# Kernel optimization log

Measured on AMD Instinct MI355X. Metric: run time of the kernel, lower is better.

The kernel has to match this reference:

```python
import jax, jax.numpy as jnp
import numpy as np

LSTM_SIZE = 64
NUM_OPS = 5
NUM_LAYERS = 7  # 2 warmup anchors + 5 sampled layers (layer_id 2..6)


def _lstm_cell(x, h, c, w_ih, w_hh, b_ih, b_hh):
    # torch LSTMCell gate order: i, f, g, o
    g = x @ w_ih.T + b_ih + h @ w_hh.T + b_hh  # [1, 4*64]
    i, f, gg, o = jnp.split(g, 4, axis=1)
    c2 = jax.nn.sigmoid(f) * c + jax.nn.sigmoid(i) * jnp.tanh(gg)
    h2 = jax.nn.sigmoid(o) * jnp.tanh(c2)
    return h2, c2


def _sampler(embed, w_ih, w_hh, b_ih, b_hh, w_soft, b_soft, b_soft_no_learn,
             w_attn1, w_attn2, v_attn, prev_c, prev_h, use_bias, key):
    keys = jax.random.split(key, 20)  # 5 layers * (2 index + 2 op) samples
    k = 0
    anchors, anchors_w1, arc_seq = [], [], []
    log_prob = jnp.float32(0.0)
    entropy = jnp.float32(0.0)
    inputs = embed[0][None, :]
    # warmup: two anchor slots (anchors are zeros, per original code)
    for _ in range(2):
        prev_h, prev_c = _lstm_cell(inputs, prev_h, prev_c, w_ih, w_hh, b_ih, b_hh)
        anchors.append(jnp.zeros((1, LSTM_SIZE), jnp.float32))
        anchors_w1.append(prev_h @ w_attn1.T)
    for layer_id in range(2, NUM_LAYERS):
        idxs, ops = [], []
        # sample 2 previous-layer indices via tiny attention
        for _ in range(2):
            prev_h, prev_c = _lstm_cell(inputs, prev_h, prev_c, w_ih, w_hh, b_ih, b_hh)
            query = jnp.concatenate(anchors_w1, axis=0)            # [layer_id, 64]
            q = jnp.tanh(query + prev_h @ w_attn2.T)               # broadcast [layer_id, 64]
            logits = (q @ v_attn.T).reshape(layer_id)              # [layer_id]
            logits = logits / 5.0 + 1.1 * jnp.tanh(logits)
            index = jax.random.categorical(keys[k], logits); k += 1
            logp = jax.nn.log_softmax(logits)
            log_prob = log_prob + (-logp[index])
            entropy = entropy + jax.lax.stop_gradient(-jnp.sum(logp * jnp.exp(logp)))
            idxs.append(index)
            A = jnp.concatenate(anchors, axis=0)                   # [layer_id, 64]
            inputs = A[index][None, :]
        # sample 2 ops
        for _ in range(2):
            prev_h, prev_c = _lstm_cell(inputs, prev_h, prev_c, w_ih, w_hh, b_ih, b_hh)
            logits = (prev_h @ w_soft.T + b_soft)                  # [1, 5]
            logits = 1.1 / 2.5 * jnp.tanh(logits / 5.0)
            if use_bias:
                logits = logits + b_soft_no_learn
            logits = logits[0]
            op_id = jax.random.categorical(keys[k], logits); k += 1
            logp = jax.nn.log_softmax(logits)
            log_prob = log_prob + (-logp[op_id])
            entropy = entropy + jax.lax.stop_gradient(-jnp.sum(logp * jnp.exp(logp)))
            ops.append(op_id)
            inputs = embed[op_id + 1][None, :]
        # extra step producing this layer's anchor
        prev_h, prev_c = _lstm_cell(inputs, prev_h, prev_c, w_ih, w_hh, b_ih, b_hh)
        anchors.append(prev_h)
        anchors_w1.append(prev_h @ w_attn1.T)
        inputs = embed[0][None, :]
        # arc layout per layer after in-place fixups: [idx1, op1, idx2, op2]
        arc_seq += [idxs[0], ops[0], idxs[1], ops[1]]
    arc = jnp.stack(arc_seq)
    return arc, entropy, log_prob, prev_c, prev_h


def setup_inputs() -> dict:
    key = jax.random.key(0)
    ks = jax.random.split(key, 9)
    u = lambda k, shape: jax.random.uniform(k, shape, jnp.float32, -0.1, 0.1)
    return {
        "embed": u(ks[0], (6, LSTM_SIZE)),
        "w_ih": u(ks[1], (4 * LSTM_SIZE, LSTM_SIZE)),
        "w_hh": u(ks[2], (4 * LSTM_SIZE, LSTM_SIZE)),
        "b_ih": u(ks[3], (4 * LSTM_SIZE,)),
        "b_hh": u(ks[4], (4 * LSTM_SIZE,)),
        "w_soft": u(ks[5], (NUM_OPS, LSTM_SIZE)),
        "b_soft": jnp.array([[10.0, 10.0, 0.0, 0.0, 0.0]], jnp.float32),
        "b_soft_no_learn": jnp.array([[0.25, 0.25, -0.25, -0.25, -0.25]], jnp.float32),
        "w_attn1": u(ks[6], (LSTM_SIZE, LSTM_SIZE)),
        "w_attn2": u(ks[7], (LSTM_SIZE, LSTM_SIZE)),
        "v_attn": u(ks[8], (1, LSTM_SIZE)),
        "seed": 0,
    }


def reference(embed, w_ih, w_hh, b_ih, b_hh, w_soft, b_soft, b_soft_no_learn,
              w_attn1, w_attn2, v_attn, seed):
    key = jax.random.key(seed)
    k1, k2 = jax.random.split(key)
    zc = jnp.zeros((1, LSTM_SIZE), jnp.float32)
    zh = jnp.zeros((1, LSTM_SIZE), jnp.float32)
    arc1, ent1, lp1, c, h = _sampler(embed, w_ih, w_hh, b_ih, b_hh, w_soft, b_soft,
                                     b_soft_no_learn, w_attn1, w_attn2, v_attn,
                                     zc, zh, True, k1)
    arc2, ent2, lp2, _, _ = _sampler(embed, w_ih, w_hh, b_ih, b_hh, w_soft, b_soft,
                                     b_soft_no_learn, w_attn1, w_attn2, v_attn,
                                     c, h, False, k2)
    return (arc1, arc2, lp1 + lp2, ent1 + ent2)
```

## Files before the change

### kernel.cpp

```cpp
#include <hip/hip_runtime.h>
#include <cstdint>

#ifndef FASTMATH
#define FASTMATH 1
#endif

#define NT 512

__device__ __forceinline__ uint32_t rotl32_(uint32_t v, int d) {
  return (v << d) | (v >> (32 - d));
}

__device__ __forceinline__ void tf2x32(uint32_t k0, uint32_t k1,
                                       uint32_t x0, uint32_t x1,
                                       uint32_t& o0, uint32_t& o1) {
  const uint32_t k2 = k0 ^ k1 ^ 0x1BD11BDAu;
  x0 += k0; x1 += k1;
#define TF4(a,b,c,d) \
  x0 += x1; x1 = rotl32_(x1,a); x1 ^= x0; \
  x0 += x1; x1 = rotl32_(x1,b); x1 ^= x0; \
  x0 += x1; x1 = rotl32_(x1,c); x1 ^= x0; \
  x0 += x1; x1 = rotl32_(x1,d); x1 ^= x0;
  TF4(13,15,26,6)
  x0 += k1; x1 += k2 + 1u;
  TF4(17,29,16,24)
  x0 += k2; x1 += k0 + 2u;
  TF4(13,15,26,6)
  x0 += k0; x1 += k1 + 3u;
  TF4(17,29,16,24)
  x0 += k1; x1 += k2 + 4u;
  TF4(13,15,26,6)
  x0 += k2; x1 += k0 + 5u;
#undef TF4
  o0 = x0; o1 = x1;
}

#if FASTMATH
__device__ __forceinline__ float tanh_(float x) {
  float e = __expf(2.0f * x);
  return 1.0f - __fdividef(2.0f, e + 1.0f);
}
__device__ __forceinline__ float sig_(float x) {
  return __fdividef(1.0f, 1.0f + __expf(-x));
}
#define log_ __logf
#define exp_ __expf
#else
__device__ __forceinline__ float tanh_(float x) { return tanhf(x); }
__device__ __forceinline__ float sig_(float x) { return 0.5f * tanhf(0.5f * x) + 0.5f; }
#define log_ logf
#define exp_ expf
#endif

template <int CTRL>
__device__ __forceinline__ float dppf(float x) {
  return __int_as_float(__builtin_amdgcn_update_dpp(
      0, __float_as_int(x), CTRL, 0xF, 0xF, true));
}
template <int CTRL>
__device__ __forceinline__ int dppi(int x) {
  return __builtin_amdgcn_update_dpp(0, x, CTRL, 0xF, 0xF, true);
}
constexpr int QP1 = 0xB1;
constexpr int QP2 = 0x4E;
constexpr int HM  = 0x141;

__global__ __launch_bounds__(NT, 2)
void nas_controller(const float* __restrict__ embed,
                    const float* __restrict__ w_ih,
                    const float* __restrict__ w_hh,
                    const float* __restrict__ b_ih,
                    const float* __restrict__ b_hh,
                    const float* __restrict__ w_soft,
                    const float* __restrict__ b_soft,
                    const float* __restrict__ b_soft_nl,
                    const float* __restrict__ w_attn1,
                    const float* __restrict__ w_attn2,
                    const float* __restrict__ v_attn,
                    const int* __restrict__ seedp,
                    float* __restrict__ out) {
  const int tid  = threadIdx.x;
  const int lane = tid & 63;
  const int wid  = tid >> 6;

  const int hh   = lane & 1;
  const int role = (lane >> 1) & 3;
  const int ul   = lane >> 3;
  const int u    = (wid << 3) | ul;
  const int rblk = (0x3120 >> (4 * role)) & 0xF;
  const int refrow = rblk * 64 + u;

  __shared__ __align__(16) float attn1L[64 * 68];
  __shared__ __align__(16) float attn2L[64 * 68];
  __shared__ __align__(16) float wsoftL[5 * 68];
  __shared__ __align__(16) float aw1sF[7 * 68];
  __shared__ __align__(16) float hw2[64];
  __shared__ __align__(16) float hL[2][64];
  __shared__ __align__(16) float preL[13 * 256];
  __shared__ float gL[320];
  __shared__ float vaL[64];
  __shared__ float bsoftL[8], bnlL[8];
  __shared__ int   seliL;

  for (int i4 = tid; i4 < 1024; i4 += NT) {
    int r = i4 >> 4, c4 = i4 & 15;
    reinterpret_cast<float4*>(attn1L)[r * 17 + c4] =
        reinterpret_cast<const float4*>(w_attn1)[i4];
    reinterpret_cast<float4*>(attn2L)[r * 17 + c4] =
        reinterpret_cast<const float4*>(w_attn2)[i4];
  }
  if (tid < 320) { int r = tid >> 6, c = tid & 63; wsoftL[r * 68 + c] = w_soft[tid]; }
  if (tid < 64) { vaL[tid] = v_attn[tid]; hL[0][tid] = 0.f; hL[1][tid] = 0.f; }
  if (tid < 8) {
    bsoftL[tid] = (tid < 5) ? b_soft[tid] : 0.f;
    bnlL[tid]   = (tid < 5) ? b_soft_nl[tid] : 0.f;
  }
  for (int i = tid; i < 512; i += NT) preL[6 * 256 + i] = 0.f;

  if (tid < 320) {
    int s = tid >= 160 ? 1 : 0;
    int rem = tid - s * 160;
    int k = rem >> 3, i = rem & 7;
    uint32_t a, b, ka, kb, o0, o1;
    tf2x32(0u, (uint32_t)seedp[0], 0u, (uint32_t)s, a, b);
    tf2x32(a, b, 0u, (uint32_t)k, ka, kb);
    tf2x32(ka, kb, 0u, (uint32_t)i, o0, o1);
    uint32_t bits = o0 ^ o1;
    const float TINY = 1.1754943508222875e-38f;
    float uu = __uint_as_float((bits >> 9) | 0x3f800000u) - 1.0f;
    uu = uu * (1.0f - TINY) + TINY;
    uu = fmaxf(TINY, uu);
    gL[tid] = -log_(-log_(uu));
  }

  float4 wi[8], wh[8];
  {
    const float4* a = reinterpret_cast<const float4*>(w_ih) + refrow * 16 + hh * 8;
#pragma unroll
    for (int j = 0; j < 8; ++j) wi[j] = a[j];
    const float4* b = reinterpret_cast<const float4*>(w_hh) + refrow * 16 + hh * 8;
#pragma unroll
    for (int j = 0; j < 8; ++j) wh[j] = b[j];
  }
  const float bsum = b_ih[refrow] + b_hh[refrow];

#pragma unroll
  for (int e = 0; e < 6; ++e) {
    const float4* x4 = reinterpret_cast<const float4*>(embed) + e * 16 + hh * 8;
    float ax = 0, ay = 0, az = 0, aw = 0;
#pragma unroll
    for (int j = 0; j < 8; ++j) {
      float4 x = x4[j], w = wi[j];
      ax = fmaf(w.x, x.x, ax); ay = fmaf(w.y, x.y, ay);
      az = fmaf(w.z, x.z, az); aw = fmaf(w.w, x.w, aw);
    }
    float acc = (ax + ay) + (az + aw);
    float tot = acc + dppf<QP1>(acc);
    if (hh == 0) preL[e * 256 + u * 4 + role] = tot;
  }

  int curH = 0, srcSlot = 0;
  float creg = 0.f;
  float lp = 0.f, ent = 0.f;

  auto lstm = [&]() {
    __syncthreads();
    const float4* h4 = reinterpret_cast<const float4*>(hL[curH]) + hh * 8;
    float ax = 0, ay = 0, az = 0, aw = 0;
#pragma unroll
    for (int j = 0; j < 8; ++j) {
      float4 x = h4[j], w = wh[j];
      ax = fmaf(w.x, x.x, ax); ay = fmaf(w.y, x.y, ay);
      az = fmaf(w.z, x.z, az); aw = fmaf(w.w, x.w, aw);
    }
    float acc = (ax + ay) + (az + aw);
    if (hh == 0) acc += preL[srcSlot * 256 + u * 4 + role] + bsum;
    float gs = acc + dppf<QP1>(acc);
    float nl = (role == 1) ? tanh_(gs) : sig_(gs);
    float other = dppf<QP2>(nl);
    float P = (lane & 4) ? (((role == 2) ? nl : other) * creg)
                         : (nl * other);
    float c2 = P + dppf<HM>(P);
    creg = c2;
    if (role == 3 && hh == 0) hL[curH ^ 1][u] = nl * tanh_(c2);
    curH ^= 1;
  };

  auto matvec = [&](const float* Wl, float* dst) {
    const int r = tid >> 3, q = tid & 7;
    const float4* w4 = reinterpret_cast<const float4*>(Wl + r * 68) + q * 2;
    float4 wa = w4[0], wb = w4[1];
    const float4* h4 = reinterpret_cast<const float4*>(hL[curH]) + q * 2;
    float4 ha = h4[0], hb = h4[1];
    float acc = fmaf(wa.x, ha.x, fmaf(wa.y, ha.y, fmaf(wa.z, ha.z, wa.w * ha.w)));
    acc += fmaf(wb.x, hb.x, fmaf(wb.y, hb.y, fmaf(wb.z, hb.z, wb.w * hb.w)));
    acc += dppf<QP1>(acc); acc += dppf<QP2>(acc); acc += dppf<HM>(acc);
    if (q == 0) dst[r] = acc;
  };

  auto anchorPre = [&](int slot) {
    const float4* h4 = reinterpret_cast<const float4*>(hL[curH]) + hh * 8;
    float ax = 0, ay = 0, az = 0, aw = 0;
#pragma unroll
    for (int j = 0; j < 8; ++j) {
      float4 x = h4[j], w = wi[j];
      ax = fmaf(w.x, x.x, ax); ay = fmaf(w.y, x.y, ay);
      az = fmaf(w.z, x.z, az); aw = fmaf(w.w, x.w, aw);
    }
    float acc = (ax + ay) + (az + aw);
    float tot = acc + dppf<QP1>(acc);
    if (hh == 0) preL[slot * 256 + u * 4 + role] = tot;
  };

  int sIdx = 0;
  auto doSample = [&](int n, int k, int mode, float raw, float* op) {
    float l;
    if (lane < n) {
      if (mode == 0) l = raw / 5.0f + 1.1f * tanh_(raw);
      else {
        l = (float)(1.1 / 2.5) * tanh_(raw / 5.0f);
        if (mode == 1) l += bnlL[lane];
      }
    } else l = -INFINITY;
    float g = (lane < n) ? gL[sIdx * 160 + k * 8 + lane] : 0.f;
    float v = (lane < n) ? (l + g) : -INFINITY;
    int bi = lane & 7;
    float lw = l;
#define ARGSTEP(C) { float ov = dppf<C>(v), ol = dppf<C>(lw); int oi = dppi<C>(bi); \
    bool t = (ov > v) || (ov == v && oi < bi); if (t) { v = ov; lw = ol; bi = oi; } }
    ARGSTEP(QP1) ARGSTEP(QP2) ARGSTEP(HM)
#undef ARGSTEP
    float mx = l;
    mx = fmaxf(mx, dppf<QP1>(mx)); mx = fmaxf(mx, dppf<QP2>(mx)); mx = fmaxf(mx, dppf<HM>(mx));
    float e = (lane < n) ? exp_(l - mx) : 0.f;
    float ss = e; ss += dppf<QP1>(ss); ss += dppf<QP2>(ss); ss += dppf<HM>(ss);
    float lse = log_(ss);
    float lpi = l - mx - lse;
    float ec = (lane < n) ? lpi * exp_(lpi) : 0.f;
    ec += dppf<QP1>(ec); ec += dppf<QP2>(ec); ec += dppf<HM>(ec);
    if (lane == 0) {
      lp  += -(lw - mx - lse);
      ent += -ec;
      seliL = bi;
      op[0] = (float)bi;
    }
  };

  __syncthreads();

  for (int s = 0; s < 2; ++s) {
    sIdx = s;
    srcSlot = 0;
    for (int w = 0; w < 2; ++w) {
      lstm();
      __syncthreads();
      matvec(attn1L, aw1sF + w * 68);
    }
    int keyk = 0;
    for (int L = 2; L <= 6; ++L) {
      for (int t = 0; t < 2; ++t) {
        lstm();
        __syncthreads();
        matvec(attn2L, hw2);
        __syncthreads();
        if (wid == 0) {
          const int g8 = lane >> 3, j = lane & 7;
          float sacc = 0.f;
          if (g8 < L) {
#pragma unroll
            for (int e2 = 0; e2 < 8; ++e2) {
              int c = j * 8 + e2;
              sacc = fmaf(tanh_(aw1sF[g8 * 68 + c] + hw2[c]), vaL[c], sacc);
            }
          }
          sacc += dppf<QP1>(sacc); sacc += dppf<QP2>(sacc); sacc += dppf<HM>(sacc);
          float raw = __shfl(sacc, lane << 3);
          doSample(L, keyk, 0, raw, out + s * 20 + (L - 2) * 4 + t * 2);
        }
        keyk++;
        __syncthreads();
        srcSlot = 6 + seliL;
      }
      for (int t = 0; t < 2; ++t) {
        lstm();
        __syncthreads();
        if (wid == 0) {
          const int g8 = lane >> 3, j = lane & 7;
          float sacc = 0.f;
          if (g8 < 5) {
#pragma unroll
            for (int e2 = 0; e2 < 8; ++e2) {
              int c = j * 8 + e2;
              sacc = fmaf(wsoftL[g8 * 68 + c], hL[curH][c], sacc);
            }
          }
          sacc += dppf<QP1>(sacc); sacc += dppf<QP2>(sacc); sacc += dppf<HM>(sacc);
          float raw = __shfl(sacc, lane << 3) + bsoftL[lane & 7];
          doSample(5, keyk, (s == 0) ? 1 : 2, raw, out + s * 20 + (L - 2) * 4 + t * 2 + 1);
        }
        keyk++;
        __syncthreads();
        srcSlot = 1 + seliL;
      }
      lstm();
      __syncthreads();
      matvec(attn1L, aw1sF + L * 68);
      anchorPre(6 + L);
      srcSlot = 0;
    }
  }

  if (tid == 0) { out[40] = lp; out[41] = ent; }
}

extern "C" void kernel_launch(void* const* d_in, const int* in_sizes, int n_in,
                              void* d_out, int out_size, void* d_ws, size_t ws_size,
                              hipStream_t stream) {
  (void)in_sizes; (void)n_in; (void)out_size; (void)d_ws; (void)ws_size;
  nas_controller<<<1, NT, 0, stream>>>(
      (const float*)d_in[0],
      (const float*)d_in[1],
      (const float*)d_in[2],
      (const float*)d_in[3],
      (const float*)d_in[4],
      (const float*)d_in[5],
      (const float*)d_in[6],
      (const float*)d_in[7],
      (const float*)d_in[8],
      (const float*)d_in[9],
      (const float*)d_in[10],
      (const int*)d_in[11],
      (float*)d_out);
}
```

Baseline: 75.48 us.

## Run the sequential LSTM sampler in a single wavefront without block barriers

```diff
diff --git a/kernel.cpp b/kernel.cpp
--- a/kernel.cpp
+++ b/kernel.cpp
@@ -5,7 +5,7 @@
 #define FASTMATH 1
 #endif
 
-#define NT 512
+#define NT 256
 
 __device__ __forceinline__ uint32_t rotl32_(uint32_t v, int d) {
   return (v << d) | (v >> (32 - d));
@@ -65,7 +65,11 @@
 constexpr int QP2 = 0x4E;
 constexpr int HM  = 0x141;
 
-__global__ __launch_bounds__(NT, 2)
+__device__ __forceinline__ float rl(float v, int l) {
+  return __int_as_float(__builtin_amdgcn_readlane(__float_as_int(v), l));
+}
+
+__global__ __launch_bounds__(NT, 1)
 void nas_controller(const float* __restrict__ embed,
                     const float* __restrict__ w_ih,
                     const float* __restrict__ w_hh,
@@ -83,46 +87,53 @@
   const int lane = tid & 63;
   const int wid  = tid >> 6;
 
-  const int hh   = lane & 1;
-  const int role = (lane >> 1) & 3;
-  const int ul   = lane >> 3;
-  const int u    = (wid << 3) | ul;
-  const int rblk = (0x3120 >> (4 * role)) & 0xF;
-  const int refrow = rblk * 64 + u;
-
-  __shared__ __align__(16) float attn1L[64 * 68];
-  __shared__ __align__(16) float attn2L[64 * 68];
-  __shared__ __align__(16) float wsoftL[5 * 68];
-  __shared__ __align__(16) float aw1sF[7 * 68];
-  __shared__ __align__(16) float hw2[64];
-  __shared__ __align__(16) float hL[2][64];
+  __shared__ __align__(16) float attn1L[4096];
+  __shared__ __align__(16) float attn2L[4096];
+  __shared__ __align__(16) float wsoftL[512];
+  __shared__ __align__(16) float vaL[64];
   __shared__ __align__(16) float preL[13 * 256];
+  __shared__ __align__(16) float aw1sL[8 * 68];
+  __shared__ __align__(16) float hw2L[64];
   __shared__ float gL[320];
-  __shared__ float vaL[64];
   __shared__ float bsoftL[8], bnlL[8];
-  __shared__ int   seliL;
-
-  for (int i4 = tid; i4 < 1024; i4 += NT) {
-    int r = i4 >> 4, c4 = i4 & 15;
-    reinterpret_cast<float4*>(attn1L)[r * 17 + c4] =
-        reinterpret_cast<const float4*>(w_attn1)[i4];
-    reinterpret_cast<float4*>(attn2L)[r * 17 + c4] =
-        reinterpret_cast<const float4*>(w_attn2)[i4];
-  }
-  if (tid < 320) { int r = tid >> 6, c = tid & 63; wsoftL[r * 68 + c] = w_soft[tid]; }
-  if (tid < 64) { vaL[tid] = v_attn[tid]; hL[0][tid] = 0.f; hL[1][tid] = 0.f; }
+
+  float4 wri[16], wrf[16], wrg[16], wro[16];
+  if (wid == 0) {
+    const float4* p = reinterpret_cast<const float4*>(w_hh);
+#pragma unroll
+    for (int k = 0; k < 16; ++k) {
+      wri[k] = p[(0 * 64 + lane) * 16 + k];
+      wrf[k] = p[(1 * 64 + lane) * 16 + k];
+      wrg[k] = p[(2 * 64 + lane) * 16 + k];
+      wro[k] = p[(3 * 64 + lane) * 16 + k];
+    }
+  }
+
+  {
+    const float4* g1 = reinterpret_cast<const float4*>(w_attn1);
+    const float4* g2 = reinterpret_cast<const float4*>(w_attn2);
+    float4* l1 = reinterpret_cast<float4*>(attn1L);
+    float4* l2 = reinterpret_cast<float4*>(attn2L);
+    for (int i4 = tid; i4 < 1024; i4 += NT) {
+      int r = i4 >> 4, c4 = i4 & 15, d = (r << 4) + (c4 ^ (r & 15));
+      l1[d] = g1[i4];
+      l2[d] = g2[i4];
+    }
+  }
+  if (tid < 512) wsoftL[tid] = (tid < 320) ? w_soft[tid] : 0.f;
+  if (tid < 64) vaL[tid] = v_attn[tid];
   if (tid < 8) {
     bsoftL[tid] = (tid < 5) ? b_soft[tid] : 0.f;
     bnlL[tid]   = (tid < 5) ? b_soft_nl[tid] : 0.f;
   }
   for (int i = tid; i < 512; i += NT) preL[6 * 256 + i] = 0.f;
 
-  if (tid < 320) {
-    int s = tid >= 160 ? 1 : 0;
-    int rem = tid - s * 160;
+  for (int t = tid; t < 320; t += NT) {
+    int s_ = (t >= 160) ? 1 : 0;
+    int rem = t - s_ * 160;
     int k = rem >> 3, i = rem & 7;
     uint32_t a, b, ka, kb, o0, o1;
-    tf2x32(0u, (uint32_t)seedp[0], 0u, (uint32_t)s, a, b);
+    tf2x32(0u, (uint32_t)seedp[0], 0u, (uint32_t)s_, a, b);
     tf2x32(a, b, 0u, (uint32_t)k, ka, kb);
     tf2x32(ka, kb, 0u, (uint32_t)i, o0, o1);
     uint32_t bits = o0 ^ o1;
@@ -130,90 +141,107 @@
     float uu = __uint_as_float((bits >> 9) | 0x3f800000u) - 1.0f;
     uu = uu * (1.0f - TINY) + TINY;
     uu = fmaxf(TINY, uu);
-    gL[tid] = -log_(-log_(uu));
-  }
-
-  float4 wi[8], wh[8];
-  {
-    const float4* a = reinterpret_cast<const float4*>(w_ih) + refrow * 16 + hh * 8;
-#pragma unroll
-    for (int j = 0; j < 8; ++j) wi[j] = a[j];
-    const float4* b = reinterpret_cast<const float4*>(w_hh) + refrow * 16 + hh * 8;
-#pragma unroll
-    for (int j = 0; j < 8; ++j) wh[j] = b[j];
-  }
-  const float bsum = b_ih[refrow] + b_hh[refrow];
-
-#pragma unroll
-  for (int e = 0; e < 6; ++e) {
-    const float4* x4 = reinterpret_cast<const float4*>(embed) + e * 16 + hh * 8;
-    float ax = 0, ay = 0, az = 0, aw = 0;
-#pragma unroll
-    for (int j = 0; j < 8; ++j) {
-      float4 x = x4[j], w = wi[j];
-      ax = fmaf(w.x, x.x, ax); ay = fmaf(w.y, x.y, ay);
-      az = fmaf(w.z, x.z, az); aw = fmaf(w.w, x.w, aw);
-    }
-    float acc = (ax + ay) + (az + aw);
-    float tot = acc + dppf<QP1>(acc);
-    if (hh == 0) preL[e * 256 + u * 4 + role] = tot;
-  }
-
-  int curH = 0, srcSlot = 0;
-  float creg = 0.f;
-  float lp = 0.f, ent = 0.f;
+    gL[t] = -log_(-log_(uu));
+  }
+
+  for (int e = wid; e < 6; e += 4) {
+    float ew = embed[e * 64 + lane];
+    const float4* q = reinterpret_cast<const float4*>(w_ih);
+    float ai = 0, af = 0, ag = 0, ao = 0;
+#pragma unroll
+    for (int c4 = 0; c4 < 16; ++c4) {
+      float4 wiv = q[(0 * 64 + lane) * 16 + c4], wfv = q[(1 * 64 + lane) * 16 + c4],
+             wgv = q[(2 * 64 + lane) * 16 + c4], wov = q[(3 * 64 + lane) * 16 + c4];
+      float s0 = rl(ew, 4 * c4), s1 = rl(ew, 4 * c4 + 1),
+            s2 = rl(ew, 4 * c4 + 2), s3 = rl(ew, 4 * c4 + 3);
+      ai = fmaf(wiv.x, s0, ai); ai = fmaf(wiv.y, s1, ai);
+      ai = fmaf(wiv.z, s2, ai); ai = fmaf(wiv.w, s3, ai);
+      af = fmaf(wfv.x, s0, af); af = fmaf(wfv.y, s1, af);
+      af = fmaf(wfv.z, s2, af); af = fmaf(wfv.w, s3, af);
+      ag = fmaf(wgv.x, s0, ag); ag = fmaf(wgv.y, s1, ag);
+      ag = fmaf(wgv.z, s2, ag); ag = fmaf(wgv.w, s3, ag);
+      ao = fmaf(wov.x, s0, ao); ao = fmaf(wov.y, s1, ao);
+      ao = fmaf(wov.z, s2, ao); ao = fmaf(wov.w, s3, ao);
+    }
+    reinterpret_cast<float4*>(preL)[e * 64 + lane] = make_float4(ai, af, ag, ao);
+  }
+
+  __syncthreads();
+  if (wid != 0) return;
+
+  const float bias_i = b_ih[lane] + b_hh[lane];
+  const float bias_f = b_ih[64 + lane] + b_hh[64 + lane];
+  const float bias_g = b_ih[128 + lane] + b_hh[128 + lane];
+  const float bias_o = b_ih[192 + lane] + b_hh[192 + lane];
+
+  float shv[64];
+#pragma unroll
+  for (int c = 0; c < 64; ++c) shv[c] = 0.f;
+  float creg = 0.f, lp = 0.f, ent = 0.f;
+  int srcSlot = 0, sIdx = 0;
 
   auto lstm = [&]() {
-    __syncthreads();
-    const float4* h4 = reinterpret_cast<const float4*>(hL[curH]) + hh * 8;
-    float ax = 0, ay = 0, az = 0, aw = 0;
-#pragma unroll
-    for (int j = 0; j < 8; ++j) {
-      float4 x = h4[j], w = wh[j];
-      ax = fmaf(w.x, x.x, ax); ay = fmaf(w.y, x.y, ay);
-      az = fmaf(w.z, x.z, az); aw = fmaf(w.w, x.w, aw);
-    }
-    float acc = (ax + ay) + (az + aw);
-    if (hh == 0) acc += preL[srcSlot * 256 + u * 4 + role] + bsum;
-    float gs = acc + dppf<QP1>(acc);
-    float nl = (role == 1) ? tanh_(gs) : sig_(gs);
-    float other = dppf<QP2>(nl);
-    float P = (lane & 4) ? (((role == 2) ? nl : other) * creg)
-                         : (nl * other);
-    float c2 = P + dppf<HM>(P);
+    float4 pre = reinterpret_cast<float4*>(preL)[srcSlot * 64 + lane];
+    float ai = 0, af = 0, ag = 0, ao = 0;
+#pragma unroll
+    for (int c4 = 0; c4 < 16; ++c4) {
+      float4 wiv = wri[c4], wfv = wrf[c4], wgv = wrg[c4], wov = wro[c4];
+      float s0 = shv[4 * c4], s1 = shv[4 * c4 + 1],
+            s2 = shv[4 * c4 + 2], s3 = shv[4 * c4 + 3];
+      ai = fmaf(wiv.x, s0, ai); ai = fmaf(wiv.y, s1, ai);
+      ai = fmaf(wiv.z, s2, ai); ai = fmaf(wiv.w, s3, ai);
+      af = fmaf(wfv.x, s0, af); af = fmaf(wfv.y, s1, af);
+      af = fmaf(wfv.z, s2, af); af = fmaf(wfv.w, s3, af);
+      ag = fmaf(wgv.x, s0, ag); ag = fmaf(wgv.y, s1, ag);
+      ag = fmaf(wgv.z, s2, ag); ag = fmaf(wgv.w, s3, ag);
+      ao = fmaf(wov.x, s0, ao); ao = fmaf(wov.y, s1, ao);
+      ao = fmaf(wov.z, s2, ao); ao = fmaf(wov.w, s3, ao);
+    }
+    float gi = ai + pre.x + bias_i, gf = af + pre.y + bias_f;
+    float gg = ag + pre.z + bias_g, go = ao + pre.w + bias_o;
+    float c2 = sig_(gf) * creg + sig_(gi) * tanh_(gg);
+    float h2 = sig_(go) * tanh_(c2);
     creg = c2;
-    if (role == 3 && hh == 0) hL[curH ^ 1][u] = nl * tanh_(c2);
-    curH ^= 1;
+#pragma unroll
+    for (int c = 0; c < 64; ++c) shv[c] = rl(h2, c);
   };
 
-  auto matvec = [&](const float* Wl, float* dst) {
-    const int r = tid >> 3, q = tid & 7;
-    const float4* w4 = reinterpret_cast<const float4*>(Wl + r * 68) + q * 2;
-    float4 wa = w4[0], wb = w4[1];
-    const float4* h4 = reinterpret_cast<const float4*>(hL[curH]) + q * 2;
-    float4 ha = h4[0], hb = h4[1];
-    float acc = fmaf(wa.x, ha.x, fmaf(wa.y, ha.y, fmaf(wa.z, ha.z, wa.w * ha.w)));
-    acc += fmaf(wb.x, hb.x, fmaf(wb.y, hb.y, fmaf(wb.z, hb.z, wb.w * hb.w)));
-    acc += dppf<QP1>(acc); acc += dppf<QP2>(acc); acc += dppf<HM>(acc);
-    if (q == 0) dst[r] = acc;
+  auto matvec = [&](const float* W) -> float {
+    const float4* w4 = reinterpret_cast<const float4*>(W);
+    float a0 = 0, a1 = 0, a2 = 0, a3 = 0;
+#pragma unroll
+    for (int c4 = 0; c4 < 16; ++c4) {
+      float4 w = w4[(lane << 4) + (c4 ^ (lane & 15))];
+      a0 = fmaf(w.x, shv[4 * c4], a0);
+      a1 = fmaf(w.y, shv[4 * c4 + 1], a1);
+      a2 = fmaf(w.z, shv[4 * c4 + 2], a2);
+      a3 = fmaf(w.w, shv[4 * c4 + 3], a3);
+    }
+    return (a0 + a1) + (a2 + a3);
   };
 
   auto anchorPre = [&](int slot) {
-    const float4* h4 = reinterpret_cast<const float4*>(hL[curH]) + hh * 8;
-    float ax = 0, ay = 0, az = 0, aw = 0;
-#pragma unroll
-    for (int j = 0; j < 8; ++j) {
-      float4 x = h4[j], w = wi[j];
-      ax = fmaf(w.x, x.x, ax); ay = fmaf(w.y, x.y, ay);
-      az = fmaf(w.z, x.z, az); aw = fmaf(w.w, x.w, aw);
-    }
-    float acc = (ax + ay) + (az + aw);
-    float tot = acc + dppf<QP1>(acc);
-    if (hh == 0) preL[slot * 256 + u * 4 + role] = tot;
+    const float4* q = reinterpret_cast<const float4*>(w_ih);
+    float ai = 0, af = 0, ag = 0, ao = 0;
+#pragma unroll
+    for (int c4 = 0; c4 < 16; ++c4) {
+      float4 wiv = q[(0 * 64 + lane) * 16 + c4], wfv = q[(1 * 64 + lane) * 16 + c4],
+             wgv = q[(2 * 64 + lane) * 16 + c4], wov = q[(3 * 64 + lane) * 16 + c4];
+      float s0 = shv[4 * c4], s1 = shv[4 * c4 + 1],
+            s2 = shv[4 * c4 + 2], s3 = shv[4 * c4 + 3];
+      ai = fmaf(wiv.x, s0, ai); ai = fmaf(wiv.y, s1, ai);
+      ai = fmaf(wiv.z, s2, ai); ai = fmaf(wiv.w, s3, ai);
+      af = fmaf(wfv.x, s0, af); af = fmaf(wfv.y, s1, af);
+      af = fmaf(wfv.z, s2, af); af = fmaf(wfv.w, s3, af);
+      ag = fmaf(wgv.x, s0, ag); ag = fmaf(wgv.y, s1, ag);
+      ag = fmaf(wgv.z, s2, ag); ag = fmaf(wgv.w, s3, ag);
+      ao = fmaf(wov.x, s0, ao); ao = fmaf(wov.y, s1, ao);
+      ao = fmaf(wov.z, s2, ao); ao = fmaf(wov.w, s3, ao);
+    }
+    reinterpret_cast<float4*>(preL)[slot * 64 + lane] = make_float4(ai, af, ag, ao);
   };
 
-  int sIdx = 0;
-  auto doSample = [&](int n, int k, int mode, float raw, float* op) {
+  auto doSample = [&](int n, int k, int mode, float raw, float* op) -> int {
     float l;
     if (lane < n) {
       if (mode == 0) l = raw / 5.0f + 1.1f * tanh_(raw);
@@ -227,7 +255,7 @@
     int bi = lane & 7;
     float lw = l;
 #define ARGSTEP(C) { float ov = dppf<C>(v), ol = dppf<C>(lw); int oi = dppi<C>(bi); \
-    bool t = (ov > v) || (ov == v && oi < bi); if (t) { v = ov; lw = ol; bi = oi; } }
+    bool tk = (ov > v) || (ov == v && oi < bi); if (tk) { v = ov; lw = ol; bi = oi; } }
     ARGSTEP(QP1) ARGSTEP(QP2) ARGSTEP(HM)
 #undef ARGSTEP
     float mx = l;
@@ -241,76 +269,71 @@
     if (lane == 0) {
       lp  += -(lw - mx - lse);
       ent += -ec;
-      seliL = bi;
       op[0] = (float)bi;
     }
+    return __builtin_amdgcn_readfirstlane(bi);
   };
-
-  __syncthreads();
 
   for (int s = 0; s < 2; ++s) {
     sIdx = s;
     srcSlot = 0;
     for (int w = 0; w < 2; ++w) {
       lstm();
-      __syncthreads();
-      matvec(attn1L, aw1sF + w * 68);
+      aw1sL[w * 68 + lane] = matvec(attn1L);
     }
     int keyk = 0;
     for (int L = 2; L <= 6; ++L) {
       for (int t = 0; t < 2; ++t) {
         lstm();
-        __syncthreads();
-        matvec(attn2L, hw2);
-        __syncthreads();
-        if (wid == 0) {
-          const int g8 = lane >> 3, j = lane & 7;
-          float sacc = 0.f;
-          if (g8 < L) {
-#pragma unroll
-            for (int e2 = 0; e2 < 8; ++e2) {
-              int c = j * 8 + e2;
-              sacc = fmaf(tanh_(aw1sF[g8 * 68 + c] + hw2[c]), vaL[c], sacc);
-            }
-          }
-          sacc += dppf<QP1>(sacc); sacc += dppf<QP2>(sacc); sacc += dppf<HM>(sacc);
-          float raw = __shfl(sacc, lane << 3);
-          doSample(L, keyk, 0, raw, out + s * 20 + (L - 2) * 4 + t * 2);
+        hw2L[lane] = matvec(attn2L);
+        const int r8 = lane >> 3, j = lane & 7;
+        float sacc = 0.f;
+        {
+          const float4* aw = reinterpret_cast<const float4*>(aw1sL + r8 * 68 + j * 8);
+          const float4* hq = reinterpret_cast<const float4*>(hw2L + j * 8);
+          const float4* vq = reinterpret_cast<const float4*>(vaL + j * 8);
+          float4 a0 = aw[0], a1 = aw[1], h0 = hq[0], h1 = hq[1], v0 = vq[0], v1 = vq[1];
+          sacc = fmaf(tanh_(a0.x + h0.x), v0.x, sacc);
+          sacc = fmaf(tanh_(a0.y + h0.y), v0.y, sacc);
+          sacc = fmaf(tanh_(a0.z + h0.z), v0.z, sacc);
+          sacc = fmaf(tanh_(a0.w + h0.w), v0.w, sacc);
+          sacc = fmaf(tanh_(a1.x + h1.x), v1.x, sacc);
+          sacc = fmaf(tanh_(a1.y + h1.y), v1.y, sacc);
+          sacc = fmaf(tanh_(a1.z + h1.z), v1.z, sacc);
+          sacc = fmaf(tanh_(a1.w + h1.w), v1.w, sacc);
         }
+        sacc += dppf<QP1>(sacc); sacc += dppf<QP2>(sacc); sacc += dppf<HM>(sacc);
+        float raw = __shfl(sacc, lane << 3);
+        int sel = doSample(L, keyk, 0, raw, out + s * 20 + (L - 2) * 4 + t * 2);
         keyk++;
-        __syncthreads();
-        srcSlot = 6 + seliL;
+        srcSlot = 6 + sel;
       }
       for (int t = 0; t < 2; ++t) {
         lstm();
-        __syncthreads();
-        if (wid == 0) {
-          const int g8 = lane >> 3, j = lane & 7;
-          float sacc = 0.f;
-          if (g8 < 5) {
-#pragma unroll
-            for (int e2 = 0; e2 < 8; ++e2) {
-              int c = j * 8 + e2;
-              sacc = fmaf(wsoftL[g8 * 68 + c], hL[curH][c], sacc);
-            }
-          }
-          sacc += dppf<QP1>(sacc); sacc += dppf<QP2>(sacc); sacc += dppf<HM>(sacc);
-          float raw = __shfl(sacc, lane << 3) + bsoftL[lane & 7];
-          doSample(5, keyk, (s == 0) ? 1 : 2, raw, out + s * 20 + (L - 2) * 4 + t * 2 + 1);
+        float a0 = 0, a1 = 0, a2 = 0, a3 = 0;
+        const float4* wq = reinterpret_cast<const float4*>(wsoftL + (lane & 7) * 64);
+#pragma unroll
+        for (int c4 = 0; c4 < 16; ++c4) {
+          float4 w = wq[c4];
+          a0 = fmaf(w.x, shv[4 * c4], a0);
+          a1 = fmaf(w.y, shv[4 * c4 + 1], a1);
+          a2 = fmaf(w.z, shv[4 * c4 + 2], a2);
+          a3 = fmaf(w.w, shv[4 * c4 + 3], a3);
         }
+        float raw = (a0 + a1) + (a2 + a3) + bsoftL[lane & 7];
+        int sel = doSample(5, keyk, (s == 0) ? 1 : 2, raw,
+                           out + s * 20 + (L - 2) * 4 + t * 2 + 1);
         keyk++;
-        __syncthreads();
-        srcSlot = 1 + seliL;
+        srcSlot = 1 + sel;
       }
       lstm();
-      __syncthreads();
-      matvec(attn1L, aw1sF + L * 68);
+      aw1sL[L * 68 + lane] = matvec(attn1L);
       anchorPre(6 + L);
       srcSlot = 0;
     }
   }
 
-  if (tid == 0) { out[40] = lp; out[41] = ent; }
+  if (lane == 0) { out[40] = lp; out[41] = ent; }
 }
 
 extern "C" void kernel_launch(void* const* d_in, const int* in_sizes, int n_in,
```

Measured after the change: 210.6 us. 2.79x slower.

## Restructure LSTM cell into row-pair gate matvec plus shared-memory cell update

Applied to the files above, without the earlier changes.

```diff
diff --git a/kernel.cpp b/kernel.cpp
--- a/kernel.cpp
+++ b/kernel.cpp
@@ -65,7 +65,7 @@
 constexpr int QP2 = 0x4E;
 constexpr int HM  = 0x141;
 
-__global__ __launch_bounds__(NT, 2)
+__global__ __launch_bounds__(NT, 1)
 void nas_controller(const float* __restrict__ embed,
                     const float* __restrict__ w_ih,
                     const float* __restrict__ w_hh,
@@ -82,25 +82,33 @@
   const int tid  = threadIdx.x;
   const int lane = tid & 63;
   const int wid  = tid >> 6;
-
-  const int hh   = lane & 1;
-  const int role = (lane >> 1) & 3;
-  const int ul   = lane >> 3;
-  const int u    = (wid << 3) | ul;
-  const int rblk = (0x3120 >> (4 * role)) & 0xF;
-  const int refrow = rblk * 64 + u;
+  const int row  = tid >> 1;
+  const int half = tid & 1;
 
   __shared__ __align__(16) float attn1L[64 * 68];
   __shared__ __align__(16) float attn2L[64 * 68];
-  __shared__ __align__(16) float wsoftL[5 * 68];
-  __shared__ __align__(16) float aw1sF[7 * 68];
-  __shared__ __align__(16) float hw2[64];
-  __shared__ __align__(16) float hL[2][64];
-  __shared__ __align__(16) float preL[13 * 256];
+  __shared__ __align__(16) float wsoftL[5 * 68 + 8];
+  __shared__ __align__(16) float vaL[64];
+  __shared__ __align__(16) float preQ[13 * 256];
+  __shared__ __align__(16) float aw1sL[8 * 68];
+  __shared__ __align__(16) float hw2L[64];
+  __shared__ __align__(16) float hB[64];
+  __shared__ float cs[64];
+  __shared__ float gates[256];
   __shared__ float gL[320];
-  __shared__ float vaL[64];
   __shared__ float bsoftL[8], bnlL[8];
   __shared__ int   seliL;
+
+  float4 wi[8], wh[8];
+  {
+    const float4* a = reinterpret_cast<const float4*>(w_ih) + row * 16 + half * 8;
+#pragma unroll
+    for (int j = 0; j < 8; ++j) wi[j] = a[j];
+    const float4* b = reinterpret_cast<const float4*>(w_hh) + row * 16 + half * 8;
+#pragma unroll
+    for (int j = 0; j < 8; ++j) wh[j] = b[j];
+  }
+  const float bsum = b_ih[row] + b_hh[row];
 
   for (int i4 = tid; i4 < 1024; i4 += NT) {
     int r = i4 >> 4, c4 = i4 & 15;
@@ -109,20 +117,23 @@
     reinterpret_cast<float4*>(attn2L)[r * 17 + c4] =
         reinterpret_cast<const float4*>(w_attn2)[i4];
   }
-  if (tid < 320) { int r = tid >> 6, c = tid & 63; wsoftL[r * 68 + c] = w_soft[tid]; }
-  if (tid < 64) { vaL[tid] = v_attn[tid]; hL[0][tid] = 0.f; hL[1][tid] = 0.f; }
+  for (int i = tid; i < 340; i += NT) {
+    int r = i / 68, c = i % 68;
+    wsoftL[i] = (c < 64) ? w_soft[r * 64 + c] : 0.f;
+  }
+  if (tid < 64) { vaL[tid] = v_attn[tid]; hB[tid] = 0.f; cs[tid] = 0.f; }
   if (tid < 8) {
     bsoftL[tid] = (tid < 5) ? b_soft[tid] : 0.f;
     bnlL[tid]   = (tid < 5) ? b_soft_nl[tid] : 0.f;
   }
-  for (int i = tid; i < 512; i += NT) preL[6 * 256 + i] = 0.f;
+  preQ[6 * 256 + tid] = 0.f;
 
   if (tid < 320) {
-    int s = tid >= 160 ? 1 : 0;
-    int rem = tid - s * 160;
+    int s_ = (tid >= 160) ? 1 : 0;
+    int rem = tid - s_ * 160;
     int k = rem >> 3, i = rem & 7;
     uint32_t a, b, ka, kb, o0, o1;
-    tf2x32(0u, (uint32_t)seedp[0], 0u, (uint32_t)s, a, b);
+    tf2x32(0u, (uint32_t)seedp[0], 0u, (uint32_t)s_, a, b);
     tf2x32(a, b, 0u, (uint32_t)k, ka, kb);
     tf2x32(ka, kb, 0u, (uint32_t)i, o0, o1);
     uint32_t bits = o0 ^ o1;
@@ -133,86 +144,77 @@
     gL[tid] = -log_(-log_(uu));
   }
 
-  float4 wi[8], wh[8];
-  {
-    const float4* a = reinterpret_cast<const float4*>(w_ih) + refrow * 16 + hh * 8;
-#pragma unroll
-    for (int j = 0; j < 8; ++j) wi[j] = a[j];
-    const float4* b = reinterpret_cast<const float4*>(w_hh) + refrow * 16 + hh * 8;
-#pragma unroll
-    for (int j = 0; j < 8; ++j) wh[j] = b[j];
-  }
-  const float bsum = b_ih[refrow] + b_hh[refrow];
-
 #pragma unroll
   for (int e = 0; e < 6; ++e) {
-    const float4* x4 = reinterpret_cast<const float4*>(embed) + e * 16 + hh * 8;
-    float ax = 0, ay = 0, az = 0, aw = 0;
+    const float4* x4 = reinterpret_cast<const float4*>(embed + e * 64) + half * 8;
+    float a0 = 0, a1 = 0, a2 = 0, a3 = 0;
 #pragma unroll
     for (int j = 0; j < 8; ++j) {
       float4 x = x4[j], w = wi[j];
-      ax = fmaf(w.x, x.x, ax); ay = fmaf(w.y, x.y, ay);
-      az = fmaf(w.z, x.z, az); aw = fmaf(w.w, x.w, aw);
-    }
-    float acc = (ax + ay) + (az + aw);
-    float tot = acc + dppf<QP1>(acc);
-    if (hh == 0) preL[e * 256 + u * 4 + role] = tot;
-  }
-
-  int curH = 0, srcSlot = 0;
-  float creg = 0.f;
+      a0 = fmaf(w.x, x.x, a0); a1 = fmaf(w.y, x.y, a1);
+      a2 = fmaf(w.z, x.z, a2); a3 = fmaf(w.w, x.w, a3);
+    }
+    float acc = (a0 + a1) + (a2 + a3);
+    acc += __shfl_xor(acc, 1);
+    if (half == 0) preQ[e * 256 + row] = acc;
+  }
+
+  __syncthreads();
+
+  const float4* hU = reinterpret_cast<const float4*>(hB);
   float lp = 0.f, ent = 0.f;
+  int srcSlot = 0, sIdx = 0;
 
   auto lstm = [&]() {
-    __syncthreads();
-    const float4* h4 = reinterpret_cast<const float4*>(hL[curH]) + hh * 8;
-    float ax = 0, ay = 0, az = 0, aw = 0;
+    const float4* h4 = reinterpret_cast<const float4*>(hB) + half * 8;
+    float a0 = 0, a1 = 0, a2 = 0, a3 = 0;
 #pragma unroll
     for (int j = 0; j < 8; ++j) {
       float4 x = h4[j], w = wh[j];
-      ax = fmaf(w.x, x.x, ax); ay = fmaf(w.y, x.y, ay);
-      az = fmaf(w.z, x.z, az); aw = fmaf(w.w, x.w, aw);
-    }
-    float acc = (ax + ay) + (az + aw);
-    if (hh == 0) acc += preL[srcSlot * 256 + u * 4 + role] + bsum;
-    float gs = acc + dppf<QP1>(acc);
-    float nl = (role == 1) ? tanh_(gs) : sig_(gs);
-    float other = dppf<QP2>(nl);
-    float P = (lane & 4) ? (((role == 2) ? nl : other) * creg)
-                         : (nl * other);
-    float c2 = P + dppf<HM>(P);
-    creg = c2;
-    if (role == 3 && hh == 0) hL[curH ^ 1][u] = nl * tanh_(c2);
-    curH ^= 1;
+      a0 = fmaf(w.x, x.x, a0); a1 = fmaf(w.y, x.y, a1);
+      a2 = fmaf(w.z, x.z, a2); a3 = fmaf(w.w, x.w, a3);
+    }
+    float acc = (a0 + a1) + (a2 + a3);
+    acc += __shfl_xor(acc, 1);
+    if (half == 0) gates[row] = acc + preQ[srcSlot * 256 + row] + bsum;
+    __syncthreads();
+    if (tid < 64) {
+      float gi = gates[tid], gf = gates[64 + tid];
+      float gg = gates[128 + tid], go = gates[192 + tid];
+      float c2 = sig_(gf) * cs[tid] + sig_(gi) * tanh_(gg);
+      float h2 = sig_(go) * tanh_(c2);
+      cs[tid] = c2; hB[tid] = h2;
+    }
   };
 
-  auto matvec = [&](const float* Wl, float* dst) {
-    const int r = tid >> 3, q = tid & 7;
-    const float4* w4 = reinterpret_cast<const float4*>(Wl + r * 68) + q * 2;
+  auto matvecAll = [&](const float* W, float* dst) {
+    const int r8 = tid >> 3, q = tid & 7;
+    const float4* w4 = reinterpret_cast<const float4*>(W + r8 * 68 + q * 8);
     float4 wa = w4[0], wb = w4[1];
-    const float4* h4 = reinterpret_cast<const float4*>(hL[curH]) + q * 2;
+    const float4* h4 = reinterpret_cast<const float4*>(hB) + q * 2;
     float4 ha = h4[0], hb = h4[1];
     float acc = fmaf(wa.x, ha.x, fmaf(wa.y, ha.y, fmaf(wa.z, ha.z, wa.w * ha.w)));
     acc += fmaf(wb.x, hb.x, fmaf(wb.y, hb.y, fmaf(wb.z, hb.z, wb.w * hb.w)));
-    acc += dppf<QP1>(acc); acc += dppf<QP2>(acc); acc += dppf<HM>(acc);
-    if (q == 0) dst[r] = acc;
+    acc += __shfl_xor(acc, 1);
+    acc += __shfl_xor(acc, 2);
+    acc += __shfl_xor(acc, 4);
+    if (q == 0) dst[r8] = acc;
   };
 
   auto anchorPre = [&](int slot) {
-    const float4* h4 = reinterpret_cast<const float4*>(hL[curH]) + hh * 8;
-    float ax = 0, ay = 0, az = 0, aw = 0;
+    const float4* h4 = reinterpret_cast<const float4*>(hB) + half * 8;
+    float a0 = 0, a1 = 0, a2 = 0, a3 = 0;
 #pragma unroll
     for (int j = 0; j < 8; ++j) {
       float4 x = h4[j], w = wi[j];
-      ax = fmaf(w.x, x.x, ax); ay = fmaf(w.y, x.y, ay);
-      az = fmaf(w.z, x.z, az); aw = fmaf(w.w, x.w, aw);
-    }
-    float acc = (ax + ay) + (az + aw);
-    float tot = acc + dppf<QP1>(acc);
-    if (hh == 0) preL[slot * 256 + u * 4 + role] = tot;
+      a0 = fmaf(w.x, x.x, a0); a1 = fmaf(w.y, x.y, a1);
+      a2 = fmaf(w.z, x.z, a2); a3 = fmaf(w.w, x.w, a3);
+    }
+    float acc = (a0 + a1) + (a2 + a3);
+    acc += __shfl_xor(acc, 1);
+    if (half == 0) preQ[slot * 256 + row] = acc;
   };
 
-  int sIdx = 0;
   auto doSample = [&](int n, int k, int mode, float raw, float* op) {
     float l;
     if (lane < n) {
@@ -227,7 +229,7 @@
     int bi = lane & 7;
     float lw = l;
 #define ARGSTEP(C) { float ov = dppf<C>(v), ol = dppf<C>(lw); int oi = dppi<C>(bi); \
-    bool t = (ov > v) || (ov == v && oi < bi); if (t) { v = ov; lw = ol; bi = oi; } }
+    bool tk = (ov > v) || (ov == v && oi < bi); if (tk) { v = ov; lw = ol; bi = oi; } }
     ARGSTEP(QP1) ARGSTEP(QP2) ARGSTEP(HM)
 #undef ARGSTEP
     float mx = l;
@@ -246,32 +248,37 @@
     }
   };
 
-  __syncthreads();
-
   for (int s = 0; s < 2; ++s) {
     sIdx = s;
     srcSlot = 0;
     for (int w = 0; w < 2; ++w) {
       lstm();
       __syncthreads();
-      matvec(attn1L, aw1sF + w * 68);
+      matvecAll(attn1L, aw1sL + w * 68);
     }
     int keyk = 0;
     for (int L = 2; L <= 6; ++L) {
       for (int t = 0; t < 2; ++t) {
         lstm();
         __syncthreads();
-        matvec(attn2L, hw2);
+        matvecAll(attn2L, hw2L);
         __syncthreads();
         if (wid == 0) {
           const int g8 = lane >> 3, j = lane & 7;
           float sacc = 0.f;
           if (g8 < L) {
-#pragma unroll
-            for (int e2 = 0; e2 < 8; ++e2) {
-              int c = j * 8 + e2;
-              sacc = fmaf(tanh_(aw1sF[g8 * 68 + c] + hw2[c]), vaL[c], sacc);
-            }
+            const float4* aw = reinterpret_cast<const float4*>(aw1sL + g8 * 68 + j * 8);
+            const float4* hq = reinterpret_cast<const float4*>(hw2L + j * 8);
+            const float4* vq = reinterpret_cast<const float4*>(vaL + j * 8);
+            float4 A0 = aw[0], A1 = aw[1], H0 = hq[0], H1 = hq[1], V0 = vq[0], V1 = vq[1];
+            sacc = fmaf(tanh_(A0.x + H0.x), V0.x, sacc);
+            sacc = fmaf(tanh_(A0.y + H0.y), V0.y, sacc);
+            sacc = fmaf(tanh_(A0.z + H0.z), V0.z, sacc);
+            sacc = fmaf(tanh_(A0.w + H0.w), V0.w, sacc);
+            sacc = fmaf(tanh_(A1.x + H1.x), V1.x, sacc);
+            sacc = fmaf(tanh_(A1.y + H1.y), V1.y, sacc);
+            sacc = fmaf(tanh_(A1.z + H1.z), V1.z, sacc);
+            sacc = fmaf(tanh_(A1.w + H1.w), V1.w, sacc);
           }
           sacc += dppf<QP1>(sacc); sacc += dppf<QP2>(sacc); sacc += dppf<HM>(sacc);
           float raw = __shfl(sacc, lane << 3);
@@ -283,20 +290,20 @@
       }
       for (int t = 0; t < 2; ++t) {
         lstm();
-        __syncthreads();
         if (wid == 0) {
           const int g8 = lane >> 3, j = lane & 7;
           float sacc = 0.f;
           if (g8 < 5) {
-#pragma unroll
-            for (int e2 = 0; e2 < 8; ++e2) {
-              int c = j * 8 + e2;
-              sacc = fmaf(wsoftL[g8 * 68 + c], hL[curH][c], sacc);
-            }
+            const float4* wq = reinterpret_cast<const float4*>(wsoftL + g8 * 68 + j * 8);
+            float4 wa = wq[0], wb = wq[1];
+            float4 ha = hU[j * 2], hb = hU[j * 2 + 1];
+            sacc = fmaf(wa.x, ha.x, fmaf(wa.y, ha.y, fmaf(wa.z, ha.z, wa.w * ha.w)));
+            sacc += fmaf(wb.x, hb.x, fmaf(wb.y, hb.y, fmaf(wb.z, hb.z, wb.w * hb.w)));
           }
           sacc += dppf<QP1>(sacc); sacc += dppf<QP2>(sacc); sacc += dppf<HM>(sacc);
           float raw = __shfl(sacc, lane << 3) + bsoftL[lane & 7];
-          doSample(5, keyk, (s == 0) ? 1 : 2, raw, out + s * 20 + (L - 2) * 4 + t * 2 + 1);
+          doSample(5, keyk, (s == 0) ? 1 : 2, raw,
+                   out + s * 20 + (L - 2) * 4 + t * 2 + 1);
         }
         keyk++;
         __syncthreads();
@@ -304,7 +311,7 @@
       }
       lstm();
       __syncthreads();
-      matvec(attn1L, aw1sF + L * 68);
+      matvecAll(attn1L, aw1sL + L * 68);
       anchorPre(6 + L);
       srcSlot = 0;
     }
```

New measurement: 74.70 us. No clear change (-1.0%).
